# Performance work log

Hardware: AMD Instinct MI355X
Metric: run time of the kernel (lower is better)

The kernel has to match this reference:

```python
import jax, jax.numpy as jnp
import numpy as np

D_MODEL = 512
D_FFN = 1024
B, N = 8, 2048


def setup_inputs() -> dict:
    key = jax.random.key(0)
    k1, k2, k3, k4, k5, k6 = jax.random.split(key, 6)
    x = jax.random.normal(k1, (B, N, D_MODEL), dtype=jnp.float32)
    interaction_mask = jax.random.randint(k2, (B, N, N), 0, 2).astype(jnp.float32)
    s1 = 1.0 / np.sqrt(D_MODEL)
    s2 = 1.0 / np.sqrt(D_FFN)
    W1 = jax.random.uniform(k3, (D_MODEL, D_FFN), jnp.float32, -s1, s1)
    b1 = jax.random.uniform(k4, (D_FFN,), jnp.float32, -s1, s1)
    W2 = jax.random.uniform(k5, (D_FFN, 3 * D_MODEL), jnp.float32, -s2, s2)
    b2 = jax.random.uniform(k6, (3 * D_MODEL,), jnp.float32, -s2, s2)
    return {"x": x, "interaction_mask": interaction_mask,
            "W1": W1, "b1": b1, "W2": W2, "b2": b2}


def reference(x, interaction_mask, W1, b1, W2, b2):
    # 2-layer FFN: Linear -> ReLU -> Linear (identity)
    h = jax.nn.relu(x @ W1 + b1)           # [B, N, d_ffn]
    kqv = h @ W2 + b2                        # [B, N, 3*d_model]
    k, q, v = jnp.split(kqv, 3, axis=-1)     # each [B, N, d_model]
    scale = D_MODEL ** -0.5
    # softmax-free scaled dot-product
    attn = jnp.einsum("bqd,bkd->bqk", q, k) * scale  # [B, N, N]
    attn = attn * interaction_mask
    return jnp.einsum("bqk,bkd->bqd", attn, v)        # [B, N, d_model]
```

## Files before the change

### kernel.cpp

```cpp
#include <hip/hip_runtime.h>
#include <hip/hip_bf16.h>

typedef __attribute__((ext_vector_type(8))) short bf16x8;
typedef __attribute__((ext_vector_type(4))) float f32x4;

#define NB 8
#define NN 2048
#define DM 512
#define DF 1024

__device__ __forceinline__ ushort f2b(float f) {
  union { __hip_bfloat16 h; ushort u; } c;
  c.h = __float2bfloat16(f);
  return c.u;
}
__device__ __forceinline__ float b2f(ushort u) {
  union { ushort u; __hip_bfloat16 h; } c;
  c.u = u;
  return __bfloat162float(c.h);
}

typedef __attribute__((address_space(1))) const void gvoid_t;
typedef __attribute__((address_space(3))) void svoid_t;
__device__ __forceinline__ void gload16(const void* g, void* s) {
  __builtin_amdgcn_global_load_lds((gvoid_t*)g, (svoid_t*)s, 16, 0, 0);
}

__device__ __forceinline__ void gemm_core_128(
    const ushort* __restrict__ A, const ushort* __restrict__ B,
    int K, int brow, int bcol, f32x4 (&acc)[4][4], ushort* smem)
{
  const int tid = threadIdx.x;
  const int w = tid >> 6, l = tid & 63;
  const int sr = (w << 3) + (l >> 3);
  const int sc = (((l & 7) ^ (l >> 3)) << 3);
  const int fr = l & 15;
  const int arow = ((w >> 1) << 6) + fr;
  const int brw  = ((w & 1) << 6) + fr;
  char* base = (char*)smem;
  char* A0 = base;          char* B0 = base + 16384;
  char* A1 = base + 32768;  char* B1 = base + 49152;

#pragma unroll
  for (int m = 0; m < 4; m++)
#pragma unroll
    for (int n = 0; n < 4; n++)
      acc[m][n] = (f32x4){0.f, 0.f, 0.f, 0.f};

  const ushort* Ap = A + (long)(brow + sr) * K + sc;
  const ushort* Bp = B + (long)(bcol + sr) * K + sc;
  const int nkt = K >> 6;

  auto stage = [&](char* Ad, char* Bd, int kt) {
#pragma unroll
    for (int i = 0; i < 4; i++) {
      gload16(Ap + (long)i * 32 * K + kt * 64, Ad + i * 4096 + (w << 10));
      gload16(Bp + (long)i * 32 * K + kt * 64, Bd + i * 4096 + (w << 10));
    }
  };
  auto compute = [&](const char* As_, const char* Bs_) {
#pragma unroll
    for (int kk = 0; kk < 2; kk++) {
      const int cx = ((((kk << 2) + (l >> 4)) ^ (l & 7)) << 4);
      bf16x8 a[4], b[4];
#pragma unroll
      for (int m = 0; m < 4; m++)
        a[m] = *(const bf16x8*)(As_ + (arow + m * 16) * 128 + cx);
#pragma unroll
      for (int n = 0; n < 4; n++)
        b[n] = *(const bf16x8*)(Bs_ + (brw + n * 16) * 128 + cx);
#pragma unroll
      for (int m = 0; m < 4; m++)
#pragma unroll
        for (int n = 0; n < 4; n++)
          acc[m][n] = __builtin_amdgcn_mfma_f32_16x16x32_bf16(a[m], b[n], acc[m][n], 0, 0, 0);
    }
  };

  stage(A0, B0, 0);
  __syncthreads();
  for (int kt = 0; kt < nkt; kt += 2) {
    stage(A1, B1, kt + 1);
    compute(A0, B0);
    __syncthreads();
    if (kt + 2 < nkt) stage(A0, B0, kt + 2);
    compute(A1, B1);
    __syncthreads();
  }
}

__device__ __forceinline__ void acc_to_lds_bf16(f32x4 (&acc)[4][4], ushort* smem) {
  const int tid = threadIdx.x, w = tid >> 6, l = tid & 63;
  const int r0l = ((w >> 1) << 6) + ((l >> 4) << 2);
  const int c0l = ((w & 1) << 6) + (l & 15);
#pragma unroll
  for (int n = 0; n < 4; n++)
#pragma unroll
    for (int m = 0; m < 4; m++)
#pragma unroll
      for (int j = 0; j < 4; j++)
        smem[(r0l + m * 16 + j) * 128 + (c0l + n * 16)] = f2b(acc[m][n][j]);
}


__global__ __launch_bounds__(256) void k_cvt(const float* __restrict__ in,
                                             ushort* __restrict__ out) {
  const long i = ((long)blockIdx.x * 256 + threadIdx.x) << 2;
  const float4 v = *(const float4*)(in + i);
  ushort4 o;
  o.x = f2b(v.x); o.y = f2b(v.y); o.z = f2b(v.z); o.w = f2b(v.w);
  *(ushort4*)(out + i) = o;
}

__device__ __forceinline__ float ld2f(const float* p, long i) { return p[i]; }
__device__ __forceinline__ float ld2f(const __hip_bfloat16* p, long i) { return __bfloat162float(p[i]); }

template <typename TIN>
__global__ __launch_bounds__(256) void k_tr(const TIN* __restrict__ in, ushort* __restrict__ out,
                                            int R, int C, long inB, long outB) {
  __shared__ float t[32][33];
  const long b = blockIdx.z;
  const TIN* ip = in + b * inB;
  ushort* op = out + b * outB;
  const int c0 = blockIdx.x << 5, r0 = blockIdx.y << 5;
  const int tx = threadIdx.x & 31, ty = threadIdx.x >> 5;
#pragma unroll
  for (int j = 0; j < 32; j += 8)
    t[ty + j][tx] = ld2f(ip, (long)(r0 + ty + j) * C + (c0 + tx));
  __syncthreads();
#pragma unroll
  for (int j = 0; j < 32; j += 8)
    op[(long)(c0 + ty + j) * R + (r0 + tx)] = f2b(t[tx][ty + j]);
}

__global__ __launch_bounds__(256) void k_gemm1(const ushort* __restrict__ xb,
                                               const ushort* __restrict__ w1t,
                                               const float* __restrict__ b1,
                                               ushort* __restrict__ hb) {
  __shared__ ushort smem[128 * 256];
  f32x4 acc[4][4];
  const int brow = blockIdx.x << 7, bcol = blockIdx.y << 7;
  gemm_core_128(xb, w1t, DM, brow, bcol, acc, smem);
  const int tid = threadIdx.x, w = tid >> 6, l = tid & 63;
  const int c0l = ((w & 1) << 6) + (l & 15);
#pragma unroll
  for (int n = 0; n < 4; n++) {
    const float bias = b1[bcol + c0l + n * 16];
#pragma unroll
    for (int m = 0; m < 4; m++)
#pragma unroll
      for (int j = 0; j < 4; j++) {
        float v = acc[m][n][j] + bias;
        acc[m][n][j] = v > 0.f ? v : 0.f;
      }
  }
  acc_to_lds_bf16(acc, smem);
  __syncthreads();
  const int rb = tid >> 4, cb = tid & 15;
#pragma unroll
  for (int i = 0; i < 8; i++) {
    const int row = i * 16 + rb;
    bf16x8 s = *(const bf16x8*)(smem + row * 128 + cb * 8);
    *(bf16x8*)(hb + (long)(brow + row) * DF + bcol + cb * 8) = s;
  }
}

__global__ __launch_bounds__(256) void k_gemm2(const ushort* __restrict__ hb,
                                               const ushort* __restrict__ w2t,
                                               const float* __restrict__ b2,
                                               ushort* __restrict__ kb,
                                               ushort* __restrict__ qb,
                                               ushort* __restrict__ vb) {
  __shared__ ushort smem[128 * 256];
  f32x4 acc[4][4];
  const int brow = blockIdx.x << 7, bcol = blockIdx.y << 7;
  gemm_core_128(hb, w2t, DF, brow, bcol, acc, smem);
  const int seg = bcol >> 9;
  ushort* dst = (seg == 0) ? kb : ((seg == 1) ? qb : vb);
  const float sc = (seg == 1) ? 0.04419417382415922f : 1.0f;
  const int tid = threadIdx.x, w = tid >> 6, l = tid & 63;
  const int c0l = ((w & 1) << 6) + (l & 15);
#pragma unroll
  for (int n = 0; n < 4; n++) {
    const float bias = b2[bcol + c0l + n * 16];
#pragma unroll
    for (int m = 0; m < 4; m++)
#pragma unroll
      for (int j = 0; j < 4; j++)
        acc[m][n][j] = (acc[m][n][j] + bias) * sc;
  }
  acc_to_lds_bf16(acc, smem);
  __syncthreads();
  const int rb = tid >> 4, cb = tid & 15;
  const int clb = bcol - (seg << 9);
#pragma unroll
  for (int i = 0; i < 8; i++) {
    const int row = i * 16 + rb;
    bf16x8 s = *(const bf16x8*)(smem + row * 128 + cb * 8);
    *(bf16x8*)(dst + (long)(brow + row) * DM + clb + cb * 8) = s;
  }
}

__global__ __launch_bounds__(512, 2) void k_qk256(const ushort* __restrict__ qb,
                                                  const ushort* __restrict__ kb,
                                                  const float* __restrict__ mask,
                                                  ushort* __restrict__ Sbuf) {
  __shared__ ushort smem[65536];
  const int bid = blockIdx.x;
  const int batch = bid & 7;
  const int tile = bid >> 3;
  const int brow = (tile & 7) << 8, bcol = (tile >> 3) << 8;
  const ushort* A = qb + (long)batch * NN * DM;
  const ushort* B = kb + (long)batch * NN * DM;
  const int K = DM;

  const int tid = threadIdx.x;
  const int w = tid >> 6, l = tid & 63;
  const int wr = w >> 2, wc = w & 3;
  const int fr = l & 15;
  char* bufbase = (char*)smem;

  f32x4 acc[8][4];
#pragma unroll
  for (int m = 0; m < 8; m++)
#pragma unroll
    for (int n = 0; n < 4; n++)
      acc[m][n] = (f32x4){0.f, 0.f, 0.f, 0.f};

  const int srow = (w << 3) + (l >> 3);
  const int sc = (((l & 7) ^ (l >> 3)) << 3);

  auto stage_half = [&](int b, int kt, int mat, int h) {
    const ushort* P = mat ? B : A;
    const int rbase = (mat ? bcol : brow) + (h << 7);
    char* dst = bufbase + (b << 16) + (mat << 15) + (h << 14) + (w << 10);
#pragma unroll
    for (int i = 0; i < 2; i++)
      gload16(P + (long)(rbase + (i << 6) + srow) * K + (kt << 6) + sc,
              dst + (i << 13));
  };

  stage_half(0, 0, 0, 0); stage_half(0, 0, 0, 1);
  stage_half(0, 0, 1, 0); stage_half(0, 0, 1, 1);
  __syncthreads();

  const int nkt = K >> 6;
  for (int kt = 0; kt < nkt; ++kt) {
    const int b = kt & 1;
    const char* cA = bufbase + (b << 16);
    const char* cB = cA + 32768;
    const bool pre = (kt + 1 < nkt);
#pragma unroll
    for (int kk = 0; kk < 2; ++kk) {
      const int cx = ((((kk << 2) + (l >> 4)) ^ (l & 7)) << 4);
      bf16x8 bfrag[4];
#pragma unroll
      for (int n = 0; n < 4; n++)
        bfrag[n] = *(const bf16x8*)(cB + ((wc << 6) + (n << 4) + fr) * 128 + cx);
#pragma unroll
      for (int mh = 0; mh < 2; ++mh) {
        if (kk == 0 && pre) {
          stage_half(b ^ 1, kt + 1, mh, 0);
          stage_half(b ^ 1, kt + 1, mh, 1);
        }
        bf16x8 afrag[4];
#pragma unroll
        for (int mi = 0; mi < 4; mi++)
          afrag[mi] = *(const bf16x8*)(cA + ((wr << 7) + (mh << 6) + (mi << 4) + fr) * 128 + cx);
        __builtin_amdgcn_s_setprio(1);
#pragma unroll
        for (int mi = 0; mi < 4; mi++)
#pragma unroll
          for (int n = 0; n < 4; n++)
            acc[mh * 4 + mi][n] =
                __builtin_amdgcn_mfma_f32_16x16x32_bf16(afrag[mi], bfrag[n], acc[mh * 4 + mi][n], 0, 0, 0);
        __builtin_amdgcn_s_setprio(0);
      }
    }
    __syncthreads();
  }

#pragma unroll
  for (int m = 0; m < 8; m++)
#pragma unroll
    for (int n = 0; n < 4; n++)
#pragma unroll
      for (int j = 0; j < 4; j++) {
        const int row = (wr << 7) + (m << 4) + ((l >> 4) << 2) + j;
        const int col = (wc << 6) + (n << 4) + fr;
        smem[row * 256 + (col ^ ((row & 7) << 3))] = f2b(acc[m][n][j]);
      }
  __syncthreads();

  const float* mk = mask + (long)batch * NN * NN;
  ushort* S = Sbuf + (long)batch * NN * NN;
  const int rr = tid >> 4, cc = tid & 15;
#pragma unroll
  for (int i = 0; i < 8; ++i) {
    const int row = (i << 5) + rr;
    const long gr = (long)(brow + row) * NN + bcol;
#pragma unroll
    for (int hf = 0; hf < 2; ++hf) {
      const int ch = (hf << 4) + cc;
      bf16x8 s = *(const bf16x8*)(smem + row * 256 + ((ch ^ (row & 7)) << 3));
      const float4 m0 = *(const float4*)(mk + gr + ch * 8);
      const float4 m1 = *(const float4*)(mk + gr + ch * 8 + 4);
      bf16x8 o;
      o[0] = (short)f2b(b2f((ushort)s[0]) * m0.x);
      o[1] = (short)f2b(b2f((ushort)s[1]) * m0.y);
      o[2] = (short)f2b(b2f((ushort)s[2]) * m0.z);
      o[3] = (short)f2b(b2f((ushort)s[3]) * m0.w);
      o[4] = (short)f2b(b2f((ushort)s[4]) * m1.x);
      o[5] = (short)f2b(b2f((ushort)s[5]) * m1.y);
      o[6] = (short)f2b(b2f((ushort)s[6]) * m1.z);
      o[7] = (short)f2b(b2f((ushort)s[7]) * m1.w);
      *(bf16x8*)(S + gr + ch * 8) = o;
    }
  }
}

__global__ __launch_bounds__(256) void k_pv(const ushort* __restrict__ Sbuf,
                                            const ushort* __restrict__ vtb,
                                            float* __restrict__ out) {
  __shared__ ushort smem[128 * 256];
  const int batch = blockIdx.z;
  const ushort* A = Sbuf + (long)batch * NN * NN;
  const ushort* Bm = vtb + (long)batch * DM * NN;
  float* op = out + (long)batch * NN * DM;
  f32x4 acc[4][4];
  const int brow = blockIdx.x << 7, bcol = blockIdx.y << 7;
  gemm_core_128(A, Bm, NN, brow, bcol, acc, smem);
  const int tid = threadIdx.x, w = tid >> 6, l = tid & 63;
  const int r0 = brow + ((w >> 1) << 6) + ((l >> 4) << 2);
  const int c0 = bcol + ((w & 1) << 6) + (l & 15);
#pragma unroll
  for (int n = 0; n < 4; n++) {
    const int c = c0 + n * 16;
#pragma unroll
    for (int m = 0; m < 4; m++) {
      const int r = r0 + m * 16;
#pragma unroll
      for (int j = 0; j < 4; j++)
        op[(long)(r + j) * DM + c] = acc[m][n][j];
    }
  }
}

extern "C" void kernel_launch(void* const* d_in, const int* in_sizes, int n_in,
                              void* d_out, int out_size, void* d_ws, size_t ws_size,
                              hipStream_t stream) {
  const float* x    = (const float*)d_in[0];
  const float* mask = (const float*)d_in[1];
  const float* W1   = (const float*)d_in[2];
  const float* b1   = (const float*)d_in[3];
  const float* W2   = (const float*)d_in[4];
  const float* b2   = (const float*)d_in[5];
  float* out = (float*)d_out;

  char* ws = (char*)d_ws;
  size_t off = 0;
  auto alloc = [&](size_t n) { char* p = ws + off; off += (n + 255) & ~(size_t)255; return p; };
  ushort* xb  = (ushort*)alloc((size_t)NB * NN * DM * 2);
  ushort* hb  = (ushort*)alloc((size_t)NB * NN * DF * 2);
  ushort* w1t = (ushort*)alloc((size_t)DF * DM * 2);
  ushort* w2t = (ushort*)alloc((size_t)3 * DM * DF * 2);
  ushort* kb  = (ushort*)alloc((size_t)NB * NN * DM * 2);
  ushort* qb  = (ushort*)alloc((size_t)NB * NN * DM * 2);
  ushort* vb  = (ushort*)alloc((size_t)NB * NN * DM * 2);
  ushort* vtb = (ushort*)alloc((size_t)NB * NN * DM * 2);
  ushort* Sbuf = (ushort*)alloc((size_t)NB * NN * NN * 2);

  k_cvt<<<dim3(8192), dim3(256), 0, stream>>>(x, xb);
  k_tr<float><<<dim3(DF / 32, DM / 32, 1), dim3(256), 0, stream>>>(W1, w1t, DM, DF, 0, 0);
  k_tr<float><<<dim3(3 * DM / 32, DF / 32, 1), dim3(256), 0, stream>>>(W2, w2t, DF, 3 * DM, 0, 0);
  k_gemm1<<<dim3(NB * NN / 128, DF / 128), dim3(256), 0, stream>>>(xb, w1t, b1, hb);
  k_gemm2<<<dim3(NB * NN / 128, 3 * DM / 128), dim3(256), 0, stream>>>(hb, w2t, b2, kb, qb, vb);
  k_tr<__hip_bfloat16><<<dim3(DM / 32, NN / 32, NB), dim3(256), 0, stream>>>(
      (const __hip_bfloat16*)vb, vtb, NN, DM, (long)NN * DM, (long)DM * NN);
  k_qk256<<<dim3(512), dim3(512), 0, stream>>>(qb, kb, mask, Sbuf);
  k_pv<<<dim3(NN / 128, DM / 128, NB), dim3(256), 0, stream>>>(Sbuf, vtb, out);
}
```

Measured before the change: 227.4 us.

## Prefetch two K-tiles ahead with explicit vmcnt waits in QK^T GEMM

Restructures the QK^T mainloop's double buffering so loads run two tiles ahead. It issues the next-next tile's global-to-LDS loads after each compute step and uses partial s_waitcnt vmcnt(8) with raw barriers instead of full __syncthreads. The aim is to keep one tile's loads in flight while the current one is computed, hiding global memory latency. The cost is that loads are now issued all at once rather than interleaved with the MFMAs. Correctness depends on the vmcnt count matching the 8 loads issued per stage.

```diff
diff --git a/kernel.cpp b/kernel.cpp
--- a/kernel.cpp
+++ b/kernel.cpp
@@ -230,26 +230,25 @@
   const int srow = (w << 3) + (l >> 3);
   const int sc = (((l & 7) ^ (l >> 3)) << 3);
 
-  auto stage_half = [&](int b, int kt, int mat, int h) {
-    const ushort* P = mat ? B : A;
-    const int rbase = (mat ? bcol : brow) + (h << 7);
-    char* dst = bufbase + (b << 16) + (mat << 15) + (h << 14) + (w << 10);
-#pragma unroll
-    for (int i = 0; i < 2; i++)
-      gload16(P + (long)(rbase + (i << 6) + srow) * K + (kt << 6) + sc,
-              dst + (i << 13));
+  auto stage_tile = [&](int b, int kt) {
+#pragma unroll
+    for (int mat = 0; mat < 2; ++mat) {
+      const ushort* P = mat ? B : A;
+      const int rbase = mat ? bcol : brow;
+#pragma unroll
+      for (int h = 0; h < 2; ++h) {
+        char* dst = bufbase + (b << 16) + (mat << 15) + (h << 14) + (w << 10);
+#pragma unroll
+        for (int i = 0; i < 2; i++)
+          gload16(P + (long)(rbase + (h << 7) + (i << 6) + srow) * K + (kt << 6) + sc,
+                  dst + (i << 13));
+      }
+    }
   };
 
-  stage_half(0, 0, 0, 0); stage_half(0, 0, 0, 1);
-  stage_half(0, 0, 1, 0); stage_half(0, 0, 1, 1);
-  __syncthreads();
-
-  const int nkt = K >> 6;
-  for (int kt = 0; kt < nkt; ++kt) {
-    const int b = kt & 1;
+  auto compute = [&](int b) {
     const char* cA = bufbase + (b << 16);
     const char* cB = cA + 32768;
-    const bool pre = (kt + 1 < nkt);
 #pragma unroll
     for (int kk = 0; kk < 2; ++kk) {
       const int cx = ((((kk << 2) + (l >> 4)) ^ (l & 7)) << 4);
@@ -259,10 +258,6 @@
         bfrag[n] = *(const bf16x8*)(cB + ((wc << 6) + (n << 4) + fr) * 128 + cx);
 #pragma unroll
       for (int mh = 0; mh < 2; ++mh) {
-        if (kk == 0 && pre) {
-          stage_half(b ^ 1, kt + 1, mh, 0);
-          stage_half(b ^ 1, kt + 1, mh, 1);
-        }
         bf16x8 afrag[4];
 #pragma unroll
         for (int mi = 0; mi < 4; mi++)
@@ -277,7 +272,25 @@
         __builtin_amdgcn_s_setprio(0);
       }
     }
-    __syncthreads();
+  };
+
+  stage_tile(0, 0);
+  stage_tile(1, 1);
+  asm volatile("s_waitcnt vmcnt(8)" ::: "memory");
+  __builtin_amdgcn_s_barrier();
+
+  const int nkt = K >> 6;
+  for (int kt = 0; kt < nkt; ++kt) {
+    const int b = kt & 1;
+    compute(b);
+    __builtin_amdgcn_s_barrier();
+    if (kt + 2 < nkt) {
+      stage_tile(b, kt + 2);
+      asm volatile("s_waitcnt vmcnt(8)" ::: "memory");
+    } else {
+      asm volatile("s_waitcnt vmcnt(0)" ::: "memory");
+    }
+    __builtin_amdgcn_s_barrier();
   }
 
 #pragma unroll
```

Result: no change. 229.6 us (+1.0%).
